# Performance work log

Measured on AMD Instinct MI355X. Metric: run time of the kernel, lower is better.

The kernel has to match this reference:

```python
import jax, jax.numpy as jnp
import numpy as np

B, S, IN, H = 64, 1024, 256, 512

def setup_inputs() -> dict:
    key = jax.random.key(0)
    ks = jax.random.split(key, 9)
    inputs = jax.random.normal(ks[0], (B, S, IN), dtype=jnp.float32)
    timestamps = jax.random.uniform(ks[1], (B, S), dtype=jnp.float32)
    input_lens = jax.random.randint(ks[2], (B,), 1, S + 1, dtype=jnp.int64)
    sc_h = 1.0 / np.sqrt(H)
    sc_i = 1.0 / np.sqrt(IN)
    # torch Linear: y = x @ W.T + b; store transposed weights [in, out]
    W_all = jax.random.uniform(ks[3], (H, 4 * H), jnp.float32, -sc_h, sc_h)
    b_all = jax.random.uniform(ks[4], (4 * H,), jnp.float32, -sc_h, sc_h)
    U_all = jax.random.uniform(ks[5], (IN, 4 * H), jnp.float32, -sc_i, sc_i)
    b_u = jax.random.uniform(ks[6], (4 * H,), jnp.float32, -sc_i, sc_i)
    W_d = jax.random.uniform(ks[7], (H, H), jnp.float32, -sc_h, sc_h)
    b_d = jax.random.uniform(ks[8], (H,), jnp.float32, -sc_h, sc_h)
    return {"inputs": inputs, "timestamps": timestamps, "input_lens": input_lens,
            "W_all": W_all, "b_all": b_all, "U_all": U_all, "b_u": b_u,
            "W_d": W_d, "b_d": b_d}

def _time_lstm(inputs, timestamps, input_lens, W_all, b_all, U_all, b_u, W_d, b_d):
    b = inputs.shape[0]
    hdim = W_d.shape[0]
    # precompute input projection once: [B,S,4H]
    x_proj = jnp.einsum('bsi,ig->bsg', inputs, U_all) + b_u
    # elapse gate: 1 / log(e + dt), [B,S,1]
    g = 1.0 / jnp.log(jnp.float32(np.e) + timestamps)

    def step(carry, xs):
        h, c = carry
        x_t, g_t = xs  # [B,4H], [B]
        c_s1 = jnp.tanh(c @ W_d + b_d)
        c_adj = c - c_s1 + c_s1 * g_t[:, None]
        outs = h @ W_all + b_all + x_t
        f, i, o, c_tmp = jnp.split(outs, 4, axis=1)
        c_new = jax.nn.sigmoid(f) * c_adj + jax.nn.sigmoid(i) * jnp.tanh(c_tmp)
        h_new = jax.nn.sigmoid(o) * jnp.tanh(c_new)
        return (h_new, c_new), (h_new, c_new)

    h0 = jnp.zeros((b, hdim), inputs.dtype)
    c0 = jnp.zeros((b, hdim), inputs.dtype)
    xs = (jnp.swapaxes(x_proj, 0, 1), jnp.swapaxes(g, 0, 1))  # time-major
    _, (h_seq, c_seq) = jax.lax.scan(step, (h0, c0), xs)
    h_seq = jnp.swapaxes(h_seq, 0, 1)  # [B,S,H]
    c_seq = jnp.swapaxes(c_seq, 0, 1)

    seq = inputs.shape[1]
    mask = (jnp.arange(seq)[None, :] < input_lens[:, None])  # [B,S]
    outputs = jnp.where(mask[:, :, None], h_seq, 0.0)  # zeros past length, like original
    last_idx = (input_lens - 1)[:, None, None]  # [B,1,1]
    last_h = jnp.take_along_axis(h_seq, jnp.broadcast_to(last_idx, (b, 1, hdim)), axis=1)[:, 0]
    last_c = jnp.take_along_axis(c_seq, jnp.broadcast_to(last_idx, (b, 1, hdim)), axis=1)[:, 0]
    return outputs, last_h, last_c

def reference(inputs, timestamps, input_lens, W_all, b_all, U_all, b_u, W_d, b_d):
    return _time_lstm(inputs, timestamps, input_lens, W_all, b_all, U_all, b_u, W_d, b_d)
```

## Files before the change

kernel.cpp:

```cpp
#include <hip/hip_runtime.h>


typedef _Float16 f16;
typedef _Float16 f16x8 __attribute__((ext_vector_type(8)));
typedef float f32x4 __attribute__((ext_vector_type(4)));

#define S_ 1024
#define IN_ 256
#define H_ 512
#define ECONST 2.718281828459045f

__device__ __forceinline__ float sigf(float x) { return 1.0f / (1.0f + __expf(-x)); }
__device__ __forceinline__ float tanh_f(float x) { return 1.0f - 2.0f / (__expf(2.0f * x) + 1.0f); }

__device__ __forceinline__ unsigned int pack_hc(float h, float c) {
    union { f16 f; unsigned short u; } ph, pc;
    ph.f = (f16)h; pc.f = (f16)c;
    return ((unsigned int)pc.u << 16) | (unsigned int)ph.u;
}

__launch_bounds__(320, 2)
__global__ void tlstm_scan(
    const float* __restrict__ inputs, const float* __restrict__ tstamps,
    const int* __restrict__ lens,
    const float* __restrict__ W_all, const float* __restrict__ b_all,
    const float* __restrict__ U_all, const float* __restrict__ b_u,
    const float* __restrict__ W_d, const float* __restrict__ b_d,
    float* __restrict__ out0, float* __restrict__ out1, float* __restrict__ out2,
    unsigned long long* __restrict__ hcbuf, unsigned int* __restrict__ flags)
{
    __shared__ __align__(16) f16 A_sm[96 * 16 * 8];
    __shared__ __align__(16) f16 C_sm[64 * 16 * 8];
    __shared__ float outs_sm[5 * 16 * 17];
    __shared__ float c_loc[16 * 16];
    __shared__ float bias_sm[5 * 16];
    __shared__ int   len_sm[16];

    const int tid    = threadIdx.x;
    const int grp    = blockIdx.x & 3;
    const int member = blockIdx.x >> 2;
    const int wave   = tid >> 6;
    const int lane   = tid & 63;
    const int q      = lane >> 4;
    const int r16    = lane & 15;
    const int j0     = member * 16;

    f16x8 bw[24];
    if (wave < 4) {
        const int col = wave * 512 + j0 + r16;
#pragma unroll
        for (int kk = 0; kk < 24; ++kk) {
            f16x8 v;
            const int kbase = kk * 32 + q * 8;
#pragma unroll
            for (int e = 0; e < 8; ++e) {
                const int k = kbase + e;
                const float w = (kk < 16) ? W_all[k * 2048 + col]
                                          : U_all[(k - 512) * 2048 + col];
                v[e] = (f16)w;
            }
            bw[kk] = v;
        }
    } else {
        const int col = j0 + r16;
#pragma unroll
        for (int kk = 0; kk < 16; ++kk) {
            f16x8 v;
            const int kbase = kk * 32 + q * 8;
#pragma unroll
            for (int e = 0; e < 8; ++e) v[e] = (f16)W_d[(kbase + e) * 512 + col];
            bw[kk] = v;
        }
#pragma unroll
        for (int kk = 16; kk < 24; ++kk) bw[kk] = bw[0];
    }

    int sl[7];
    int ns = 0;
    for (int s = wave; s < 32; s += 5)
        if (s != member) sl[ns++] = s;

    {
        uint4 z; z.x = z.y = z.z = z.w = 0u;
        uint4* a4 = (uint4*)A_sm;
        uint4* c4 = (uint4*)C_sm;
        for (int i = tid; i < 1024; i += 320) { a4[i] = z; c4[i] = z; }
        if (tid < 256) c_loc[tid] = 0.0f;
        if (tid < 64) {
            const int w = tid >> 4, n = tid & 15;
            const int col = w * 512 + j0 + n;
            bias_sm[w * 16 + n] = b_all[col] + b_u[col];
        } else if (tid < 80) {
            const int n = tid & 15;
            bias_sm[64 + n] = b_d[j0 + n];
        }
        if (tid < 16) len_sm[tid] = lens[grp * 16 + tid];
        for (int idx = tid; idx < 1024; idx += 320) {
            const int b = idx >> 6;
            const int kx0 = (idx & 63) << 2;
            const float4 v = *(const float4*)&inputs[(((size_t)(grp * 16 + b)) * S_ + 0) * IN_ + kx0];
            union { f16 h[4]; uint2 u; } p;
            p.h[0] = (f16)v.x; p.h[1] = (f16)v.y; p.h[2] = (f16)v.z; p.h[3] = (f16)v.w;
            const int kb = 64 + (kx0 >> 3), e = kx0 & 7;
            *(uint2*)&A_sm[(kb * 16 + b) * 8 + e] = p.u;
        }
    }
    __syncthreads();

    unsigned long long* const hc_g = hcbuf + (size_t)grp * 2 * 4096;
    unsigned int* const flg = flags + grp * 32;

    for (int t = 0; t < S_; ++t) {
        float ts = 0.0f;
        if (tid < 256) {
            const int gb = grp * 16 + (tid >> 4);
            ts = tstamps[(size_t)gb * S_ + t];
        }

        f32x4 acc0 = {0.f, 0.f, 0.f, 0.f}, acc1 = {0.f, 0.f, 0.f, 0.f};
        if (wave < 4) {
            const f16* abase = &A_sm[(q * 16 + r16) * 8];
#pragma unroll
            for (int kk = 0; kk < 24; ++kk) {
                const f16x8 a = *(const f16x8*)(abase + kk * 512);
                if (kk & 1) acc1 = __builtin_amdgcn_mfma_f32_16x16x32_f16(a, bw[kk], acc1, 0, 0, 0);
                else        acc0 = __builtin_amdgcn_mfma_f32_16x16x32_f16(a, bw[kk], acc0, 0, 0, 0);
            }
        } else {
            const f16* abase = &C_sm[(q * 16 + r16) * 8];
#pragma unroll
            for (int kk = 0; kk < 16; ++kk) {
                const f16x8 a = *(const f16x8*)(abase + kk * 512);
                if (kk & 1) acc1 = __builtin_amdgcn_mfma_f32_16x16x32_f16(a, bw[kk], acc1, 0, 0, 0);
                else        acc0 = __builtin_amdgcn_mfma_f32_16x16x32_f16(a, bw[kk], acc0, 0, 0, 0);
            }
        }
        const f32x4 acc = acc0 + acc1;
#pragma unroll
        for (int r = 0; r < 4; ++r)
            outs_sm[(wave * 16 + q * 4 + r) * 17 + r16] = acc[r];
        __syncthreads();

        if (tid < 256) {
            const int b = tid >> 4, jj = tid & 15;
            const int gb = grp * 16 + b;
            const float f  = outs_sm[(0 * 16 + b) * 17 + jj] + bias_sm[0  + jj];
            const float i_ = outs_sm[(1 * 16 + b) * 17 + jj] + bias_sm[16 + jj];
            const float o  = outs_sm[(2 * 16 + b) * 17 + jj] + bias_sm[32 + jj];
            const float ct = outs_sm[(3 * 16 + b) * 17 + jj] + bias_sm[48 + jj];
            const float d  = outs_sm[(4 * 16 + b) * 17 + jj] + bias_sm[64 + jj];
            const float gt = 1.0f / __logf(ECONST + ts);
            const float cs1   = tanh_f(d);
            const float cprev = c_loc[tid];
            const float cadj  = cprev - cs1 + cs1 * gt;
            const float cnew  = sigf(f) * cadj + sigf(i_) * tanh_f(ct);
            const float hnew  = sigf(o) * tanh_f(cnew);
            c_loc[tid] = cnew;
            const int col = j0 + jj;
            const int len = len_sm[b];
            out0[((size_t)gb * S_ + t) * H_ + col] = (t < len) ? hnew : 0.0f;
            if (t == len - 1) {
                out1[gb * H_ + col] = hnew;
                out2[gb * H_ + col] = cnew;
            }
            const int fi = ((col >> 3) * 16 + b) * 8 + (col & 7);
            ((f16*)A_sm)[fi] = (f16)hnew;
            ((f16*)C_sm)[fi] = (f16)cnew;
            unsigned int* dw = (unsigned int*)(hc_g + (size_t)(t & 1) * 4096);
            __hip_atomic_store(dw + member * 256 + tid, pack_hc(hnew, cnew),
                               __ATOMIC_RELAXED, __HIP_MEMORY_SCOPE_AGENT);
        }
        __syncthreads();

        if (t < S_ - 1) {
            const unsigned int tag = (unsigned int)(t + 1);
            if (tid == 0)
                __hip_atomic_store(&flg[member], tag,
                                   __ATOMIC_RELAXED, __HIP_MEMORY_SCOPE_AGENT);

            float4 xv[4];
            if (tid < 256) {
#pragma unroll
                for (int k2 = 0; k2 < 4; ++k2) {
                    const int idx = k2 * 256 + tid;
                    const int b = idx >> 6;
                    const int kx0 = (idx & 63) << 2;
                    xv[k2] = *(const float4*)&inputs[(((size_t)(grp * 16 + b)) * S_ + (t + 1)) * IN_ + kx0];
                }
            }

            for (;;) {
                unsigned int fl = tag;
                if (lane < ns)
                    fl = __hip_atomic_load(&flg[sl[lane]],
                                           __ATOMIC_RELAXED, __HIP_MEMORY_SCOPE_AGENT);
                if (__ballot(fl >= tag) == ~0ull) break;
            }

            const unsigned long long* src = hc_g + (size_t)(t & 1) * 4096;
            unsigned long long v[7][2];
#pragma unroll
            for (int u = 0; u < 7; ++u) {
                if (u < ns) {
                    const int s = sl[u];
                    v[u][0] = __hip_atomic_load(src + s * 128 + lane,
                                                __ATOMIC_RELAXED, __HIP_MEMORY_SCOPE_AGENT);
                    v[u][1] = __hip_atomic_load(src + s * 128 + 64 + lane,
                                                __ATOMIC_RELAXED, __HIP_MEMORY_SCOPE_AGENT);
                }
            }
#pragma unroll
            for (int u = 0; u < 7; ++u) {
                if (u < ns) {
                    const int s = sl[u];
#pragma unroll
                    for (int dd = 0; dd < 2; ++dd) {
                        const int j = dd * 64 + lane;
                        const int b = j >> 3;
                        const int colL = (j & 7) * 2;
                        const int col = s * 16 + colL;
                        const unsigned long long qv = v[u][dd];
                        const unsigned int d0 = (unsigned int)qv;
                        const unsigned int d1 = (unsigned int)(qv >> 32);
                        const unsigned int hpair = (d0 & 0xFFFFu) | (d1 << 16);
                        const unsigned int cpair = (d0 >> 16) | (d1 & 0xFFFF0000u);
                        const int fi = ((col >> 3) * 16 + b) * 8 + (col & 7);
                        *(unsigned int*)((f16*)A_sm + fi) = hpair;
                        *(unsigned int*)((f16*)C_sm + fi) = cpair;
                    }
                }
            }

            if (tid < 256) {
#pragma unroll
                for (int k2 = 0; k2 < 4; ++k2) {
                    const int idx = k2 * 256 + tid;
                    const int b = idx >> 6;
                    const int kx0 = (idx & 63) << 2;
                    union { f16 h[4]; uint2 u; } p;
                    p.h[0] = (f16)xv[k2].x; p.h[1] = (f16)xv[k2].y;
                    p.h[2] = (f16)xv[k2].z; p.h[3] = (f16)xv[k2].w;
                    const int kb = 64 + (kx0 >> 3), e = kx0 & 7;
                    *(uint2*)&A_sm[(kb * 16 + b) * 8 + e] = p.u;
                }
            }
            __syncthreads();
        }
    }
}

extern "C" void kernel_launch(void* const* d_in, const int* in_sizes, int n_in,
                              void* d_out, int out_size, void* d_ws, size_t ws_size,
                              hipStream_t stream) {
    const float* inputs  = (const float*)d_in[0];
    const float* tstamps = (const float*)d_in[1];
    const int*   lens    = (const int*)d_in[2];
    const float* W_all   = (const float*)d_in[3];
    const float* b_all   = (const float*)d_in[4];
    const float* U_all   = (const float*)d_in[5];
    const float* b_u     = (const float*)d_in[6];
    const float* W_d     = (const float*)d_in[7];
    const float* b_d     = (const float*)d_in[8];

    float* out0 = (float*)d_out;
    float* out1 = out0 + (size_t)64 * 1024 * 512;
    float* out2 = out1 + (size_t)64 * 512;

    char* ws = (char*)d_ws;
    unsigned int* flags = (unsigned int*)ws;
    unsigned long long* hcbuf = (unsigned long long*)(ws + 1024);

    hipMemsetAsync(ws, 0, 1024, stream);

    tlstm_scan<<<dim3(128), dim3(320), 0, stream>>>(
        inputs, tstamps, lens, W_all, b_all, U_all, b_u, W_d, b_d,
        out0, out1, out2, hcbuf, flags);
}
```

Measured before the change: 3.491 ms.

## Embed step tags in exchanged h/c words to replace flag-based inter-block sync

Each thread now writes its packed h/c pair together with a step tag as one 64-bit atomic store. Consumers poll the data words directly until every tag matches the current step. This removes the separate flag store, the flag-polling loop, one block-wide barrier per step and the workspace memset, cutting latency on the serial recurrence's cross-block handoff. The cost is a larger exchange buffer and more polling traffic. Because the workspace is no longer cleared, stale tags left by a previous launch could match late steps and cause a race.

```diff
diff --git a/kernel.cpp b/kernel.cpp
--- a/kernel.cpp
+++ b/kernel.cpp
@@ -27,7 +27,7 @@
     const float* __restrict__ U_all, const float* __restrict__ b_u,
     const float* __restrict__ W_d, const float* __restrict__ b_d,
     float* __restrict__ out0, float* __restrict__ out1, float* __restrict__ out2,
-    unsigned long long* __restrict__ hcbuf, unsigned int* __restrict__ flags)
+    unsigned long long* __restrict__ hcbuf)
 {
     __shared__ __align__(16) f16 A_sm[96 * 16 * 8];
     __shared__ __align__(16) f16 C_sm[64 * 16 * 8];
@@ -107,8 +107,7 @@
     }
     __syncthreads();
 
-    unsigned long long* const hc_g = hcbuf + (size_t)grp * 2 * 4096;
-    unsigned int* const flg = flags + grp * 32;
+    unsigned long long* const hc_g = hcbuf + (size_t)grp * 2 * 8192;
 
     for (int t = 0; t < S_; ++t) {
         float ts = 0.0f;
@@ -155,6 +154,11 @@
             const float cadj  = cprev - cs1 + cs1 * gt;
             const float cnew  = sigf(f) * cadj + sigf(i_) * tanh_f(ct);
             const float hnew  = sigf(o) * tanh_f(cnew);
+            const unsigned long long qv =
+                ((unsigned long long)(unsigned int)(t + 1) << 32) |
+                (unsigned long long)pack_hc(hnew, cnew);
+            __hip_atomic_store(hc_g + (size_t)(t & 1) * 8192 + member * 256 + tid, qv,
+                               __ATOMIC_RELAXED, __HIP_MEMORY_SCOPE_AGENT);
             c_loc[tid] = cnew;
             const int col = j0 + jj;
             const int len = len_sm[b];
@@ -166,18 +170,11 @@
             const int fi = ((col >> 3) * 16 + b) * 8 + (col & 7);
             ((f16*)A_sm)[fi] = (f16)hnew;
             ((f16*)C_sm)[fi] = (f16)cnew;
-            unsigned int* dw = (unsigned int*)(hc_g + (size_t)(t & 1) * 4096);
-            __hip_atomic_store(dw + member * 256 + tid, pack_hc(hnew, cnew),
-                               __ATOMIC_RELAXED, __HIP_MEMORY_SCOPE_AGENT);
-        }
-        __syncthreads();
+        }
+
+        asm volatile("" ::: "memory");
 
         if (t < S_ - 1) {
-            const unsigned int tag = (unsigned int)(t + 1);
-            if (tid == 0)
-                __hip_atomic_store(&flg[member], tag,
-                                   __ATOMIC_RELAXED, __HIP_MEMORY_SCOPE_AGENT);
-
             float4 xv[4];
             if (tid < 256) {
 #pragma unroll
@@ -189,45 +186,54 @@
                 }
             }
 
-            for (;;) {
-                unsigned int fl = tag;
-                if (lane < ns)
-                    fl = __hip_atomic_load(&flg[sl[lane]],
-                                           __ATOMIC_RELAXED, __HIP_MEMORY_SCOPE_AGENT);
-                if (__ballot(fl >= tag) == ~0ull) break;
-            }
-
-            const unsigned long long* src = hc_g + (size_t)(t & 1) * 4096;
-            unsigned long long v[7][2];
+            const unsigned long long* src = hc_g + (size_t)(t & 1) * 8192;
+            const unsigned int tag = (unsigned int)(t + 1);
+            const int jb = lane * 4;
+            unsigned long long v[7][4];
+            unsigned int pend = (1u << (4 * ns)) - 1u;
+            do {
+#pragma unroll
+                for (int u = 0; u < 7; ++u) {
+                    if (u < ns) {
+                        const unsigned long long* sb = src + sl[u] * 256 + jb;
+#pragma unroll
+                        for (int k = 0; k < 4; ++k)
+                            if ((pend >> (u * 4 + k)) & 1u)
+                                v[u][k] = __hip_atomic_load(sb + k, __ATOMIC_RELAXED,
+                                                            __HIP_MEMORY_SCOPE_AGENT);
+                    }
+                }
+#pragma unroll
+                for (int u = 0; u < 7; ++u) {
+                    if (u < ns) {
+#pragma unroll
+                        for (int k = 0; k < 4; ++k)
+                            if (((pend >> (u * 4 + k)) & 1u) &&
+                                (unsigned int)(v[u][k] >> 32) == tag)
+                                pend &= ~(1u << (u * 4 + k));
+                    }
+                }
+            } while (__ballot(pend != 0u) != 0ull);
+
+            const int ub  = lane >> 2;
+            const int uc4 = (lane & 3) * 4;
 #pragma unroll
             for (int u = 0; u < 7; ++u) {
                 if (u < ns) {
                     const int s = sl[u];
-                    v[u][0] = __hip_atomic_load(src + s * 128 + lane,
-                                                __ATOMIC_RELAXED, __HIP_MEMORY_SCOPE_AGENT);
-                    v[u][1] = __hip_atomic_load(src + s * 128 + 64 + lane,
-                                                __ATOMIC_RELAXED, __HIP_MEMORY_SCOPE_AGENT);
-                }
-            }
-#pragma unroll
-            for (int u = 0; u < 7; ++u) {
-                if (u < ns) {
-                    const int s = sl[u];
-#pragma unroll
-                    for (int dd = 0; dd < 2; ++dd) {
-                        const int j = dd * 64 + lane;
-                        const int b = j >> 3;
-                        const int colL = (j & 7) * 2;
-                        const int col = s * 16 + colL;
-                        const unsigned long long qv = v[u][dd];
-                        const unsigned int d0 = (unsigned int)qv;
-                        const unsigned int d1 = (unsigned int)(qv >> 32);
-                        const unsigned int hpair = (d0 & 0xFFFFu) | (d1 << 16);
-                        const unsigned int cpair = (d0 >> 16) | (d1 & 0xFFFF0000u);
-                        const int fi = ((col >> 3) * 16 + b) * 8 + (col & 7);
-                        *(unsigned int*)((f16*)A_sm + fi) = hpair;
-                        *(unsigned int*)((f16*)C_sm + fi) = cpair;
-                    }
+                    const unsigned int p0 = (unsigned int)v[u][0];
+                    const unsigned int p1 = (unsigned int)v[u][1];
+                    const unsigned int p2 = (unsigned int)v[u][2];
+                    const unsigned int p3 = (unsigned int)v[u][3];
+                    const int col = s * 16 + uc4;
+                    const int fi  = ((col >> 3) * 16 + ub) * 8 + (col & 7);
+                    uint2 hp, cp;
+                    hp.x = (p0 & 0xFFFFu) | (p1 << 16);
+                    hp.y = (p2 & 0xFFFFu) | (p3 << 16);
+                    cp.x = (p0 >> 16) | (p1 & 0xFFFF0000u);
+                    cp.y = (p2 >> 16) | (p3 & 0xFFFF0000u);
+                    *(uint2*)((f16*)A_sm + fi) = hp;
+                    *(uint2*)((f16*)C_sm + fi) = cp;
                 }
             }
 
@@ -266,13 +272,9 @@
     float* out1 = out0 + (size_t)64 * 1024 * 512;
     float* out2 = out1 + (size_t)64 * 512;
 
-    char* ws = (char*)d_ws;
-    unsigned int* flags = (unsigned int*)ws;
-    unsigned long long* hcbuf = (unsigned long long*)(ws + 1024);
-
-    hipMemsetAsync(ws, 0, 1024, stream);
+    unsigned long long* hcbuf = (unsigned long long*)d_ws;
 
     tlstm_scan<<<dim3(128), dim3(320), 0, stream>>>(
         inputs, tstamps, lens, W_all, b_all, U_all, b_u, W_d, b_d,
-        out0, out1, out2, hcbuf, flags);
+        out0, out1, out2, hcbuf);
 }
```

New measurement: 5.839 ms. +67.3%, slower.

## Precompute next-step input projection off critical path and use per-wave ready flags

Applied to the files above, without the earlier changes.

Moves the input-projection MFMAs (x_t @ U) out of the serial recurrence step: the x part for step t+1 is computed right after the gate update, before waiting on peer blocks, and the input tile is double-buffered in a separate shared array, prefetched two steps ahead. It also removes the block-wide barrier before signalling: each wave waits on its own global stores and publishes a per-wave flag, so consumers poll four flags per peer. This shortens the per-timestep dependency chain between blocks, at the cost of more flag traffic, extra shared memory and subtler memory-ordering assumptions.

```diff
diff --git a/kernel.cpp b/kernel.cpp
--- a/kernel.cpp
+++ b/kernel.cpp
@@ -29,8 +29,9 @@
     float* __restrict__ out0, float* __restrict__ out1, float* __restrict__ out2,
     unsigned long long* __restrict__ hcbuf, unsigned int* __restrict__ flags)
 {
-    __shared__ __align__(16) f16 A_sm[96 * 16 * 8];
+    __shared__ __align__(16) f16 A_sm[64 * 16 * 8];
     __shared__ __align__(16) f16 C_sm[64 * 16 * 8];
+    __shared__ __align__(16) f16 X_sm[2][32 * 16 * 8];
     __shared__ float outs_sm[5 * 16 * 17];
     __shared__ float c_loc[16 * 16];
     __shared__ float bias_sm[5 * 16];
@@ -101,14 +102,51 @@
             const float4 v = *(const float4*)&inputs[(((size_t)(grp * 16 + b)) * S_ + 0) * IN_ + kx0];
             union { f16 h[4]; uint2 u; } p;
             p.h[0] = (f16)v.x; p.h[1] = (f16)v.y; p.h[2] = (f16)v.z; p.h[3] = (f16)v.w;
-            const int kb = 64 + (kx0 >> 3), e = kx0 & 7;
-            *(uint2*)&A_sm[(kb * 16 + b) * 8 + e] = p.u;
+            const int kb = kx0 >> 3, e = kx0 & 7;
+            *(uint2*)&X_sm[0][(kb * 16 + b) * 8 + e] = p.u;
         }
     }
     __syncthreads();
 
+    f32x4 accx0 = {0.f, 0.f, 0.f, 0.f}, accx1 = {0.f, 0.f, 0.f, 0.f};
+    {
+        float4 xv1[4];
+        if (tid < 256) {
+#pragma unroll
+            for (int k2 = 0; k2 < 4; ++k2) {
+                const int idx = k2 * 256 + tid;
+                const int b = idx >> 6;
+                const int kx0 = (idx & 63) << 2;
+                xv1[k2] = *(const float4*)&inputs[(((size_t)(grp * 16 + b)) * S_ + 1) * IN_ + kx0];
+            }
+        }
+        if (wave < 4) {
+            const f16* xb = &X_sm[0][(q * 16 + r16) * 8];
+#pragma unroll
+            for (int kx = 0; kx < 8; ++kx) {
+                const f16x8 a = *(const f16x8*)(xb + kx * 512);
+                if (kx & 1) accx1 = __builtin_amdgcn_mfma_f32_16x16x32_f16(a, bw[16 + kx], accx1, 0, 0, 0);
+                else        accx0 = __builtin_amdgcn_mfma_f32_16x16x32_f16(a, bw[16 + kx], accx0, 0, 0, 0);
+            }
+        }
+        if (tid < 256) {
+#pragma unroll
+            for (int k2 = 0; k2 < 4; ++k2) {
+                const int idx = k2 * 256 + tid;
+                const int b = idx >> 6;
+                const int kx0 = (idx & 63) << 2;
+                union { f16 h[4]; uint2 u; } p;
+                p.h[0] = (f16)xv1[k2].x; p.h[1] = (f16)xv1[k2].y;
+                p.h[2] = (f16)xv1[k2].z; p.h[3] = (f16)xv1[k2].w;
+                const int kb = kx0 >> 3, e = kx0 & 7;
+                *(uint2*)&X_sm[1][(kb * 16 + b) * 8 + e] = p.u;
+            }
+        }
+    }
+    __syncthreads();
+
     unsigned long long* const hc_g = hcbuf + (size_t)grp * 2 * 4096;
-    unsigned int* const flg = flags + grp * 32;
+    unsigned int* const flg = flags + grp * 128;
 
     for (int t = 0; t < S_; ++t) {
         float ts = 0.0f;
@@ -117,16 +155,18 @@
             ts = tstamps[(size_t)gb * S_ + t];
         }
 
-        f32x4 acc0 = {0.f, 0.f, 0.f, 0.f}, acc1 = {0.f, 0.f, 0.f, 0.f};
+        f32x4 acc0, acc1;
         if (wave < 4) {
+            acc0 = accx0; acc1 = accx1;
             const f16* abase = &A_sm[(q * 16 + r16) * 8];
 #pragma unroll
-            for (int kk = 0; kk < 24; ++kk) {
+            for (int kk = 0; kk < 16; ++kk) {
                 const f16x8 a = *(const f16x8*)(abase + kk * 512);
                 if (kk & 1) acc1 = __builtin_amdgcn_mfma_f32_16x16x32_f16(a, bw[kk], acc1, 0, 0, 0);
                 else        acc0 = __builtin_amdgcn_mfma_f32_16x16x32_f16(a, bw[kk], acc0, 0, 0, 0);
             }
         } else {
+            acc0 = (f32x4){0.f, 0.f, 0.f, 0.f}; acc1 = acc0;
             const f16* abase = &C_sm[(q * 16 + r16) * 8];
 #pragma unroll
             for (int kk = 0; kk < 16; ++kk) {
@@ -156,43 +196,56 @@
             const float cnew  = sigf(f) * cadj + sigf(i_) * tanh_f(ct);
             const float hnew  = sigf(o) * tanh_f(cnew);
             c_loc[tid] = cnew;
+            unsigned int* dw = (unsigned int*)(hc_g + (size_t)(t & 1) * 4096);
+            __hip_atomic_store(dw + member * 256 + tid, pack_hc(hnew, cnew),
+                               __ATOMIC_RELAXED, __HIP_MEMORY_SCOPE_AGENT);
             const int col = j0 + jj;
+            const int fi = ((col >> 3) * 16 + b) * 8 + (col & 7);
+            ((f16*)A_sm)[fi] = (f16)hnew;
+            ((f16*)C_sm)[fi] = (f16)cnew;
+            asm volatile("s_waitcnt vmcnt(0)" ::: "memory");
+            if ((tid & 63) == 0)
+                __hip_atomic_store(&flg[member * 4 + wave], (unsigned int)(t + 1),
+                                   __ATOMIC_RELAXED, __HIP_MEMORY_SCOPE_AGENT);
             const int len = len_sm[b];
             out0[((size_t)gb * S_ + t) * H_ + col] = (t < len) ? hnew : 0.0f;
             if (t == len - 1) {
                 out1[gb * H_ + col] = hnew;
                 out2[gb * H_ + col] = cnew;
             }
-            const int fi = ((col >> 3) * 16 + b) * 8 + (col & 7);
-            ((f16*)A_sm)[fi] = (f16)hnew;
-            ((f16*)C_sm)[fi] = (f16)cnew;
-            unsigned int* dw = (unsigned int*)(hc_g + (size_t)(t & 1) * 4096);
-            __hip_atomic_store(dw + member * 256 + tid, pack_hc(hnew, cnew),
-                               __ATOMIC_RELAXED, __HIP_MEMORY_SCOPE_AGENT);
-        }
-        __syncthreads();
+        }
+        asm volatile("" ::: "memory");
 
         if (t < S_ - 1) {
-            const unsigned int tag = (unsigned int)(t + 1);
-            if (tid == 0)
-                __hip_atomic_store(&flg[member], tag,
-                                   __ATOMIC_RELAXED, __HIP_MEMORY_SCOPE_AGENT);
-
+            if (wave < 4) {
+                const f16* xb = &X_sm[(t + 1) & 1][(q * 16 + r16) * 8];
+                f32x4 ax0 = {0.f, 0.f, 0.f, 0.f}, ax1 = {0.f, 0.f, 0.f, 0.f};
+#pragma unroll
+                for (int kx = 0; kx < 8; ++kx) {
+                    const f16x8 a = *(const f16x8*)(xb + kx * 512);
+                    if (kx & 1) ax1 = __builtin_amdgcn_mfma_f32_16x16x32_f16(a, bw[16 + kx], ax1, 0, 0, 0);
+                    else        ax0 = __builtin_amdgcn_mfma_f32_16x16x32_f16(a, bw[16 + kx], ax0, 0, 0, 0);
+                }
+                accx0 = ax0; accx1 = ax1;
+            }
+
+            const bool ldx = (t + 2 < S_);
             float4 xv[4];
-            if (tid < 256) {
+            if (ldx && tid < 256) {
 #pragma unroll
                 for (int k2 = 0; k2 < 4; ++k2) {
                     const int idx = k2 * 256 + tid;
                     const int b = idx >> 6;
                     const int kx0 = (idx & 63) << 2;
-                    xv[k2] = *(const float4*)&inputs[(((size_t)(grp * 16 + b)) * S_ + (t + 1)) * IN_ + kx0];
-                }
-            }
-
+                    xv[k2] = *(const float4*)&inputs[(((size_t)(grp * 16 + b)) * S_ + (t + 2)) * IN_ + kx0];
+                }
+            }
+
+            const unsigned int tag = (unsigned int)(t + 1);
             for (;;) {
                 unsigned int fl = tag;
-                if (lane < ns)
-                    fl = __hip_atomic_load(&flg[sl[lane]],
+                if (lane < 4 * ns)
+                    fl = __hip_atomic_load(&flg[sl[lane >> 2] * 4 + (lane & 3)],
                                            __ATOMIC_RELAXED, __HIP_MEMORY_SCOPE_AGENT);
                 if (__ballot(fl >= tag) == ~0ull) break;
             }
@@ -231,7 +284,7 @@
                 }
             }
 
-            if (tid < 256) {
+            if (ldx && tid < 256) {
 #pragma unroll
                 for (int k2 = 0; k2 < 4; ++k2) {
                     const int idx = k2 * 256 + tid;
@@ -240,8 +293,8 @@
                     union { f16 h[4]; uint2 u; } p;
                     p.h[0] = (f16)xv[k2].x; p.h[1] = (f16)xv[k2].y;
                     p.h[2] = (f16)xv[k2].z; p.h[3] = (f16)xv[k2].w;
-                    const int kb = 64 + (kx0 >> 3), e = kx0 & 7;
-                    *(uint2*)&A_sm[(kb * 16 + b) * 8 + e] = p.u;
+                    const int kb = kx0 >> 3, e = kx0 & 7;
+                    *(uint2*)&X_sm[t & 1][(kb * 16 + b) * 8 + e] = p.u;
                 }
             }
             __syncthreads();
@@ -268,9 +321,9 @@
 
     char* ws = (char*)d_ws;
     unsigned int* flags = (unsigned int*)ws;
-    unsigned long long* hcbuf = (unsigned long long*)(ws + 1024);
-
-    hipMemsetAsync(ws, 0, 1024, stream);
+    unsigned long long* hcbuf = (unsigned long long*)(ws + 2048);
+
+    hipMemsetAsync(ws, 0, 2048, stream);
 
     tlstm_scan<<<dim3(128), dim3(320), 0, stream>>>(
         inputs, tstamps, lens, W_all, b_all, U_all, b_u, W_d, b_d,
```

After: 4.569 ms. 1.31x slower.

## Split the recurrent scan over 16 wider blocks per group instead of 32

Applied to the files above, without the earlier changes.

Each cooperating block now owns 32 hidden columns with 640 threads (10 waves), so a batch group spans 16 blocks rather than 32 and the grid drops from 128 to 64 blocks. This halves the number of peers each block has to poll flags for and exchange h/c state with every timestep. The exchange is also reworked to use vectorised 128-bit shared-memory writes. In exchange each block does more MFMA and elementwise work per step, and only half as many CUs take part.

```diff
diff --git a/kernel.cpp b/kernel.cpp
--- a/kernel.cpp
+++ b/kernel.cpp
@@ -19,7 +19,7 @@
     return ((unsigned int)pc.u << 16) | (unsigned int)ph.u;
 }
 
-__launch_bounds__(320, 2)
+__launch_bounds__(640, 1)
 __global__ void tlstm_scan(
     const float* __restrict__ inputs, const float* __restrict__ tstamps,
     const int* __restrict__ lens,
@@ -27,13 +27,13 @@
     const float* __restrict__ U_all, const float* __restrict__ b_u,
     const float* __restrict__ W_d, const float* __restrict__ b_d,
     float* __restrict__ out0, float* __restrict__ out1, float* __restrict__ out2,
-    unsigned long long* __restrict__ hcbuf, unsigned int* __restrict__ flags)
+    unsigned int* __restrict__ hcbuf, unsigned int* __restrict__ flags)
 {
     __shared__ __align__(16) f16 A_sm[96 * 16 * 8];
     __shared__ __align__(16) f16 C_sm[64 * 16 * 8];
-    __shared__ float outs_sm[5 * 16 * 17];
-    __shared__ float c_loc[16 * 16];
-    __shared__ float bias_sm[5 * 16];
+    __shared__ float outs_sm[5 * 16 * 33];
+    __shared__ float c_loc[16 * 32];
+    __shared__ float bias_sm[5 * 32];
     __shared__ int   len_sm[16];
 
     const int tid    = threadIdx.x;
@@ -43,11 +43,11 @@
     const int lane   = tid & 63;
     const int q      = lane >> 4;
     const int r16    = lane & 15;
-    const int j0     = member * 16;
+    const int j0     = member * 32;
 
     f16x8 bw[24];
-    if (wave < 4) {
-        const int col = wave * 512 + j0 + r16;
+    if (wave < 8) {
+        const int col = (wave >> 1) * 512 + j0 + (wave & 1) * 16 + r16;
 #pragma unroll
         for (int kk = 0; kk < 24; ++kk) {
             f16x8 v;
@@ -62,7 +62,7 @@
             bw[kk] = v;
         }
     } else {
-        const int col = j0 + r16;
+        const int col = j0 + (wave & 1) * 16 + r16;
 #pragma unroll
         for (int kk = 0; kk < 16; ++kk) {
             f16x8 v;
@@ -75,27 +75,26 @@
         for (int kk = 16; kk < 24; ++kk) bw[kk] = bw[0];
     }
 
-    int sl[7];
+    int sl[2];
     int ns = 0;
-    for (int s = wave; s < 32; s += 5)
+    for (int s = wave; s < 16; s += 10)
         if (s != member) sl[ns++] = s;
 
     {
         uint4 z; z.x = z.y = z.z = z.w = 0u;
         uint4* a4 = (uint4*)A_sm;
         uint4* c4 = (uint4*)C_sm;
-        for (int i = tid; i < 1024; i += 320) { a4[i] = z; c4[i] = z; }
-        if (tid < 256) c_loc[tid] = 0.0f;
-        if (tid < 64) {
-            const int w = tid >> 4, n = tid & 15;
+        for (int i = tid; i < 1024; i += 640) { a4[i] = z; c4[i] = z; }
+        if (tid < 512) c_loc[tid] = 0.0f;
+        if (tid < 128) {
+            const int w = tid >> 5, n = tid & 31;
             const int col = w * 512 + j0 + n;
-            bias_sm[w * 16 + n] = b_all[col] + b_u[col];
-        } else if (tid < 80) {
-            const int n = tid & 15;
-            bias_sm[64 + n] = b_d[j0 + n];
+            bias_sm[tid] = b_all[col] + b_u[col];
+        } else if (tid < 160) {
+            bias_sm[tid] = b_d[j0 + (tid & 31)];
         }
         if (tid < 16) len_sm[tid] = lens[grp * 16 + tid];
-        for (int idx = tid; idx < 1024; idx += 320) {
+        for (int idx = tid; idx < 1024; idx += 640) {
             const int b = idx >> 6;
             const int kx0 = (idx & 63) << 2;
             const float4 v = *(const float4*)&inputs[(((size_t)(grp * 16 + b)) * S_ + 0) * IN_ + kx0];
@@ -107,18 +106,18 @@
     }
     __syncthreads();
 
-    unsigned long long* const hc_g = hcbuf + (size_t)grp * 2 * 4096;
-    unsigned int* const flg = flags + grp * 32;
+    unsigned int* const hc_g = hcbuf + (size_t)grp * 2 * 8192;
+    unsigned int* const flg = flags + grp * 16;
 
     for (int t = 0; t < S_; ++t) {
         float ts = 0.0f;
-        if (tid < 256) {
-            const int gb = grp * 16 + (tid >> 4);
+        if (tid < 512) {
+            const int gb = grp * 16 + (tid >> 5);
             ts = tstamps[(size_t)gb * S_ + t];
         }
 
         f32x4 acc0 = {0.f, 0.f, 0.f, 0.f}, acc1 = {0.f, 0.f, 0.f, 0.f};
-        if (wave < 4) {
+        if (wave < 8) {
             const f16* abase = &A_sm[(q * 16 + r16) * 8];
 #pragma unroll
             for (int kk = 0; kk < 24; ++kk) {
@@ -136,19 +135,23 @@
             }
         }
         const f32x4 acc = acc0 + acc1;
-#pragma unroll
-        for (int r = 0; r < 4; ++r)
-            outs_sm[(wave * 16 + q * 4 + r) * 17 + r16] = acc[r];
+        {
+            const int grow = (wave < 8) ? (wave >> 1) : 4;
+            const int ncol = (wave & 1) * 16 + r16;
+#pragma unroll
+            for (int r = 0; r < 4; ++r)
+                outs_sm[(grow * 16 + q * 4 + r) * 33 + ncol] = acc[r];
+        }
         __syncthreads();
 
-        if (tid < 256) {
-            const int b = tid >> 4, jj = tid & 15;
+        if (tid < 512) {
+            const int b = tid >> 5, jj = tid & 31;
             const int gb = grp * 16 + b;
-            const float f  = outs_sm[(0 * 16 + b) * 17 + jj] + bias_sm[0  + jj];
-            const float i_ = outs_sm[(1 * 16 + b) * 17 + jj] + bias_sm[16 + jj];
-            const float o  = outs_sm[(2 * 16 + b) * 17 + jj] + bias_sm[32 + jj];
-            const float ct = outs_sm[(3 * 16 + b) * 17 + jj] + bias_sm[48 + jj];
-            const float d  = outs_sm[(4 * 16 + b) * 17 + jj] + bias_sm[64 + jj];
+            const float f  = outs_sm[(0 * 16 + b) * 33 + jj] + bias_sm[0   + jj];
+            const float i_ = outs_sm[(1 * 16 + b) * 33 + jj] + bias_sm[32  + jj];
+            const float o  = outs_sm[(2 * 16 + b) * 33 + jj] + bias_sm[64  + jj];
+            const float ct = outs_sm[(3 * 16 + b) * 33 + jj] + bias_sm[96  + jj];
+            const float d  = outs_sm[(4 * 16 + b) * 33 + jj] + bias_sm[128 + jj];
             const float gt = 1.0f / __logf(ECONST + ts);
             const float cs1   = tanh_f(d);
             const float cprev = c_loc[tid];
@@ -166,8 +169,8 @@
             const int fi = ((col >> 3) * 16 + b) * 8 + (col & 7);
             ((f16*)A_sm)[fi] = (f16)hnew;
             ((f16*)C_sm)[fi] = (f16)cnew;
-            unsigned int* dw = (unsigned int*)(hc_g + (size_t)(t & 1) * 4096);
-            __hip_atomic_store(dw + member * 256 + tid, pack_hc(hnew, cnew),
+            __hip_atomic_store(hc_g + (t & 1) * 8192 + member * 512 + tid,
+                               pack_hc(hnew, cnew),
                                __ATOMIC_RELAXED, __HIP_MEMORY_SCOPE_AGENT);
         }
         __syncthreads();
@@ -178,11 +181,11 @@
                 __hip_atomic_store(&flg[member], tag,
                                    __ATOMIC_RELAXED, __HIP_MEMORY_SCOPE_AGENT);
 
-            float4 xv[4];
-            if (tid < 256) {
-#pragma unroll
-                for (int k2 = 0; k2 < 4; ++k2) {
-                    const int idx = k2 * 256 + tid;
+            float4 xv[2];
+            if (tid < 512) {
+#pragma unroll
+                for (int k2 = 0; k2 < 2; ++k2) {
+                    const int idx = k2 * 512 + tid;
                     const int b = idx >> 6;
                     const int kx0 = (idx & 63) << 2;
                     xv[k2] = *(const float4*)&inputs[(((size_t)(grp * 16 + b)) * S_ + (t + 1)) * IN_ + kx0];
@@ -197,44 +200,62 @@
                 if (__ballot(fl >= tag) == ~0ull) break;
             }
 
-            const unsigned long long* src = hc_g + (size_t)(t & 1) * 4096;
-            unsigned long long v[7][2];
-#pragma unroll
-            for (int u = 0; u < 7; ++u) {
+            const unsigned long long* src =
+                (const unsigned long long*)(hc_g + (t & 1) * 8192);
+            unsigned long long v[2][4];
+#pragma unroll
+            for (int u = 0; u < 2; ++u) {
                 if (u < ns) {
-                    const int s = sl[u];
-                    v[u][0] = __hip_atomic_load(src + s * 128 + lane,
-                                                __ATOMIC_RELAXED, __HIP_MEMORY_SCOPE_AGENT);
-                    v[u][1] = __hip_atomic_load(src + s * 128 + 64 + lane,
-                                                __ATOMIC_RELAXED, __HIP_MEMORY_SCOPE_AGENT);
-                }
-            }
-#pragma unroll
-            for (int u = 0; u < 7; ++u) {
-                if (u < ns) {
-                    const int s = sl[u];
-#pragma unroll
-                    for (int dd = 0; dd < 2; ++dd) {
-                        const int j = dd * 64 + lane;
-                        const int b = j >> 3;
-                        const int colL = (j & 7) * 2;
-                        const int col = s * 16 + colL;
-                        const unsigned long long qv = v[u][dd];
-                        const unsigned int d0 = (unsigned int)qv;
-                        const unsigned int d1 = (unsigned int)(qv >> 32);
-                        const unsigned int hpair = (d0 & 0xFFFFu) | (d1 << 16);
-                        const unsigned int cpair = (d0 >> 16) | (d1 & 0xFFFF0000u);
-                        const int fi = ((col >> 3) * 16 + b) * 8 + (col & 7);
-                        *(unsigned int*)((f16*)A_sm + fi) = hpair;
-                        *(unsigned int*)((f16*)C_sm + fi) = cpair;
+                    const unsigned long long* sb = src + sl[u] * 256 + lane * 4;
+#pragma unroll
+                    for (int k = 0; k < 4; ++k)
+                        v[u][k] = __hip_atomic_load(sb + k, __ATOMIC_RELAXED,
+                                                    __HIP_MEMORY_SCOPE_AGENT);
+                }
+            }
+            {
+                const int ub  = lane >> 2;
+                const int uc8 = (lane & 3) * 8;
+#pragma unroll
+                for (int u = 0; u < 2; ++u) {
+                    if (u < ns) {
+                        const int col0 = sl[u] * 32 + uc8;
+                        const int fi0  = ((col0 >> 3) * 16 + ub) * 8;
+                        uint4 hp, cp;
+                        {
+                            const unsigned int d0 = (unsigned int)v[u][0];
+                            const unsigned int d1 = (unsigned int)(v[u][0] >> 32);
+                            hp.x = (d0 & 0xFFFFu) | (d1 << 16);
+                            cp.x = (d0 >> 16) | (d1 & 0xFFFF0000u);
+                        }
+                        {
+                            const unsigned int d0 = (unsigned int)v[u][1];
+                            const unsigned int d1 = (unsigned int)(v[u][1] >> 32);
+                            hp.y = (d0 & 0xFFFFu) | (d1 << 16);
+                            cp.y = (d0 >> 16) | (d1 & 0xFFFF0000u);
+                        }
+                        {
+                            const unsigned int d0 = (unsigned int)v[u][2];
+                            const unsigned int d1 = (unsigned int)(v[u][2] >> 32);
+                            hp.z = (d0 & 0xFFFFu) | (d1 << 16);
+                            cp.z = (d0 >> 16) | (d1 & 0xFFFF0000u);
+                        }
+                        {
+                            const unsigned int d0 = (unsigned int)v[u][3];
+                            const unsigned int d1 = (unsigned int)(v[u][3] >> 32);
+                            hp.w = (d0 & 0xFFFFu) | (d1 << 16);
+                            cp.w = (d0 >> 16) | (d1 & 0xFFFF0000u);
+                        }
+                        *(uint4*)((f16*)A_sm + fi0) = hp;
+                        *(uint4*)((f16*)C_sm + fi0) = cp;
                     }
                 }
             }
 
-            if (tid < 256) {
-#pragma unroll
-                for (int k2 = 0; k2 < 4; ++k2) {
-                    const int idx = k2 * 256 + tid;
+            if (tid < 512) {
+#pragma unroll
+                for (int k2 = 0; k2 < 2; ++k2) {
+                    const int idx = k2 * 512 + tid;
                     const int b = idx >> 6;
                     const int kx0 = (idx & 63) << 2;
                     union { f16 h[4]; uint2 u; } p;
@@ -268,11 +289,11 @@
 
     char* ws = (char*)d_ws;
     unsigned int* flags = (unsigned int*)ws;
-    unsigned long long* hcbuf = (unsigned long long*)(ws + 1024);
+    unsigned int* hcbuf = (unsigned int*)(ws + 1024);
 
     hipMemsetAsync(ws, 0, 1024, stream);
 
-    tlstm_scan<<<dim3(128), dim3(320), 0, stream>>>(
+    tlstm_scan<<<dim3(64), dim3(640), 0, stream>>>(
         inputs, tstamps, lens, W_all, b_all, U_all, b_u, W_d, b_d,
         out0, out1, out2, hcbuf, flags);
 }
```

Result: slower. 3.873 ms (+10.9%).
